# Performance work log

Measured on AMD Instinct MI355X. Metric: run time of the kernel, lower is better.

Reference implementation:

```python
import jax, jax.numpy as jnp
import numpy as np

N_HEAD, D_MODEL, D_K, D_V = 16, 1024, 64, 64
BIAS_WEIGHT = 1.0
NEG = -10000.0


def setup_inputs() -> dict:
    key = jax.random.key(0)
    ks = jax.random.split(key, 9)
    B, L = 2, 2048
    q = jax.random.normal(ks[0], (B, L, D_MODEL), dtype=jnp.float32)
    k = jax.random.normal(ks[1], (B, L, D_MODEL), dtype=jnp.float32)
    v = jax.random.normal(ks[2], (B, L, D_MODEL), dtype=jnp.float32)
    mask = jax.random.randint(ks[3], (B, L, L), 0, 2, dtype=jnp.int32)
    bias = jax.random.normal(ks[4], (B, L, L), dtype=jnp.float32)
    s = 1.0 / np.sqrt(D_MODEL)
    w_qs = jax.random.uniform(ks[5], (D_MODEL, N_HEAD * D_K), jnp.float32, -s, s)
    w_ks = jax.random.uniform(ks[6], (D_MODEL, N_HEAD * D_K), jnp.float32, -s, s)
    w_vs = jax.random.uniform(ks[7], (D_MODEL, N_HEAD * D_V), jnp.float32, -s, s)
    w_fc = jax.random.uniform(ks[8], (N_HEAD * D_V, D_MODEL), jnp.float32, -s, s)
    return {"q": q, "k": k, "v": v, "mask": mask, "bias": bias,
            "w_qs": w_qs, "w_ks": w_ks, "w_vs": w_vs, "w_fc": w_fc}


def reference(q, k, v, mask, bias, w_qs, w_ks, w_vs, w_fc):
    B, Lq, _ = q.shape
    # project and split heads: [B, H, L, d]
    qh = (q @ w_qs).reshape(B, Lq, N_HEAD, D_K).transpose(0, 2, 1, 3)
    kh = (k @ w_ks).reshape(B, k.shape[1], N_HEAD, D_K).transpose(0, 2, 1, 3)
    vh = (v @ w_vs).reshape(B, v.shape[1], N_HEAD, D_V).transpose(0, 2, 1, 3)
    temperature = D_K ** 0.5
    attn = jnp.einsum('bhqd,bhkd->bhqk', qh / temperature, kh)
    attn = attn + bias[:, None, :, :] * BIAS_WEIGHT
    attn = jnp.where(mask[:, None, :, :] == 0, NEG, attn)
    attn = jax.nn.softmax(attn, axis=-1)
    out = jnp.einsum('bhqk,bhkd->bhqd', attn, vh)
    out = out.transpose(0, 2, 1, 3).reshape(B, Lq, N_HEAD * D_V)
    return out @ w_fc
```

## Files before the change

kernel.cpp:

```cpp
#include <hip/hip_runtime.h>
#include <cstddef>

#define DEV static __device__ __forceinline__

typedef float f32x4 __attribute__((ext_vector_type(4)));
typedef __bf16 bf16x8 __attribute__((ext_vector_type(8)));
typedef __bf16 bf16x4v __attribute__((ext_vector_type(4)));
typedef unsigned short u16x8 __attribute__((ext_vector_type(8)));
typedef unsigned short u16x4 __attribute__((ext_vector_type(4)));
typedef unsigned u32x2 __attribute__((ext_vector_type(2)));
typedef unsigned u32x4 __attribute__((ext_vector_type(4)));
typedef _Float16 f16;
typedef _Float16 f16x4 __attribute__((ext_vector_type(4)));

constexpr int BB = 2, LL = 2048, DM = 1024, NH = 16, DK = 64;
constexpr float LOG2E = 1.44269504f;

DEV unsigned short f2bf(float f) {
  unsigned u = __builtin_bit_cast(unsigned, f);
  u += 0x7fffu + ((u >> 16) & 1u);
  return (unsigned short)(u >> 16);
}
DEV u16x4 cvt4(f32x4 v) {
  bf16x4v b = __builtin_convertvector(v, bf16x4v);
  return __builtin_bit_cast(u16x4, b);
}
DEV bf16x8 asbf(u16x8 v) { return __builtin_bit_cast(bf16x8, v); }
DEV f32x4 mfma16(u16x8 a, u16x8 b, f32x4 c) {
  return __builtin_amdgcn_mfma_f32_16x16x32_bf16(asbf(a), asbf(b), c, 0, 0, 0);
}
#if __has_builtin(__builtin_amdgcn_exp2f)
DEV float fexp2(float x) { return __builtin_amdgcn_exp2f(x); }
#else
DEV float fexp2(float x) { return exp2f(x); }
#endif
DEV void swap32(unsigned& a, unsigned& b) {
#if __has_builtin(__builtin_amdgcn_permlane32_swap)
  u32x2 r = __builtin_amdgcn_permlane32_swap(a, b, false, false);
  a = r[0]; b = r[1];
#else
  asm("v_permlane32_swap_b32 %0, %1" : "+v"(a), "+v"(b));
#endif
}
DEV void swap16(unsigned& a, unsigned& b) {
#if __has_builtin(__builtin_amdgcn_permlane16_swap)
  u32x2 r = __builtin_amdgcn_permlane16_swap(a, b, false, false);
  a = r[0]; b = r[1];
#else
  asm("v_permlane16_swap_b32 %0, %1" : "+v"(a), "+v"(b));
#endif
}
DEV void g2lds16(const void* g, void* l) {
  __builtin_amdgcn_global_load_lds(
      (const __attribute__((address_space(1))) unsigned int*)g,
      (__attribute__((address_space(3))) unsigned int*)l, 16, 0, 0);
}

__global__ __launch_bounds__(256) void prep_w(const float* __restrict__ w0,
                                              const float* __restrict__ w1,
                                              const float* __restrict__ w2,
                                              const float* __restrict__ w3,
                                              unsigned short* __restrict__ wT) {
  __shared__ float tile[32][33];
  int z = blockIdx.z;
  const float* W = (z == 0) ? w0 : (z == 1) ? w1 : (z == 2) ? w2 : w3;
  unsigned short* out = wT + (size_t)z * DM * DM;
  int k0 = blockIdx.y * 32, n0 = blockIdx.x * 32;
  int tx = threadIdx.x, ty = threadIdx.y;
#pragma unroll
  for (int p = 0; p < 4; p++)
    tile[ty + 8 * p][tx] = W[(size_t)(k0 + ty + 8 * p) * DM + n0 + tx];
  __syncthreads();
#pragma unroll
  for (int p = 0; p < 4; p++)
    out[(size_t)(n0 + ty + 8 * p) * DM + k0 + tx] = f2bf(tile[tx][ty + 8 * p]);
}

__global__ __launch_bounds__(256) void prep_bm(const int* __restrict__ mask,
                                               const float* __restrict__ bias,
                                               f16* __restrict__ bmf) {
  int t = threadIdx.x, w = t >> 6, lane = t & 63;
  int bq = blockIdx.y;
  int kt = blockIdx.x * 4 + w;
  int b = bq >> 7, qt = bq & 127;
  int q = qt * 16 + (lane & 15);
  int k = kt * 16 + (lane >> 4) * 4;
  size_t src = ((size_t)b * LL + q) * LL + k;
  int4 mk = *(const int4*)(mask + src);
  float4 bs = *(const float4*)(bias + src);
  f16x4 o;
  o[0] = (f16)((mk.x == 0 ? -10000.f : bs.x) * LOG2E);
  o[1] = (f16)((mk.y == 0 ? -10000.f : bs.y) * LOG2E);
  o[2] = (f16)((mk.z == 0 ? -10000.f : bs.z) * LOG2E);
  o[3] = (f16)((mk.w == 0 ? -10000.f : bs.w) * LOG2E);
  *(f16x4*)(bmf + ((size_t)bq * 128 + kt) * 256 + lane * 4) = o;
}

__global__ __launch_bounds__(256) void prep_cvt(const float* __restrict__ s0,
                                                const float* __restrict__ s1,
                                                const float* __restrict__ s2,
                                                unsigned short* __restrict__ dst) {
  int z = blockIdx.y;
  const float* src = (z == 0) ? s0 : (z == 1) ? s1 : s2;
  size_t i = ((size_t)blockIdx.x * 256 + threadIdx.x) * 8;
  float4 a = *(const float4*)(src + i);
  float4 b = *(const float4*)(src + i + 4);
  u16x8 o;
  o[0] = f2bf(a.x); o[1] = f2bf(a.y); o[2] = f2bf(a.z); o[3] = f2bf(a.w);
  o[4] = f2bf(b.x); o[5] = f2bf(b.y); o[6] = f2bf(b.z); o[7] = f2bf(b.w);
  *(u16x8*)(dst + (size_t)z * (size_t)(BB * LL) * DM + i) = o;
}

template <int KITERS>
DEV void gemm_core(const unsigned short* __restrict__ A,
                   const unsigned short* __restrict__ BT,
                   unsigned short (*Al)[128 * 64], unsigned short (*Bl)[128 * 64],
                   int m0, int n0, int k0beg, int t, f32x4 (&acc)[4][4]) {
  int lane = t & 63, c = lane & 15, qd = lane >> 4;
  int w = t >> 6, wm = w >> 1, wn = w & 1;
  int r0 = t >> 3;
  int gsw = (t & 7) ^ (r0 & 7);
  u16x8 ar[4], br[4];

  auto load_tile = [&](int k0) {
#pragma unroll
    for (int p = 0; p < 4; ++p) {
      ar[p] = *(const u16x8*)&A[(size_t)(m0 + 32 * p + r0) * DM + k0 + 8 * gsw];
      br[p] = *(const u16x8*)&BT[(size_t)(n0 + 32 * p + r0) * DM + k0 + 8 * gsw];
    }
  };
  auto store_tile = [&](int buf) {
#pragma unroll
    for (int p = 0; p < 4; ++p) {
      *(u16x8*)&Al[buf][p * 2048 + t * 8] = ar[p];
      *(u16x8*)&Bl[buf][p * 2048 + t * 8] = br[p];
    }
  };
  auto compute = [&](int buf) {
#pragma unroll
    for (int ks = 0; ks < 2; ++ks) {
      u16x8 af[4], bfr[4];
#pragma unroll
      for (int mt = 0; mt < 4; ++mt)
        af[mt] = *(const u16x8*)&Al[buf][(64 * wm + 16 * mt + c) * 64 +
                                         (((4 * ks + qd) ^ (c & 7)) << 3)];
#pragma unroll
      for (int nt = 0; nt < 4; ++nt)
        bfr[nt] = *(const u16x8*)&Bl[buf][(64 * wn + 16 * nt + c) * 64 +
                                          (((4 * ks + qd) ^ (c & 7)) << 3)];
#pragma unroll
      for (int mt = 0; mt < 4; ++mt)
#pragma unroll
        for (int nt = 0; nt < 4; ++nt)
          acc[mt][nt] = mfma16(af[mt], bfr[nt], acc[mt][nt]);
    }
  };

  load_tile(k0beg);
  store_tile(0);
  __syncthreads();
#pragma unroll 1
  for (int kk = 0; kk < KITERS; ++kk) {
    if (kk + 1 < KITERS) load_tile(k0beg + (kk + 1) * 64);
    compute(kk & 1);
    if (kk + 1 < KITERS) store_tile((kk + 1) & 1);
    __syncthreads();
  }
}

__global__ __launch_bounds__(256) void proj_gemm(const unsigned short* __restrict__ qkvb,
                                                 const unsigned short* __restrict__ wT,
                                                 unsigned short* __restrict__ qh,
                                                 unsigned short* __restrict__ kh,
                                                 unsigned short* __restrict__ vT) {
  __shared__ unsigned short Al[2][128 * 64];
  __shared__ unsigned short Bl[2][128 * 64];
  int z = blockIdx.z;
  const unsigned short* A = qkvb + (size_t)z * BB * LL * DM;
  const unsigned short* BT = wT + (size_t)z * DM * DM;
  int t = threadIdx.x, lane = t & 63, c = lane & 15, qd = lane >> 4;
  int w = t >> 6, wm = w >> 1, wn = w & 1;
  int m0 = blockIdx.y * 128, n0 = blockIdx.x * 128;
  f32x4 acc[4][4] = {};
  gemm_core<DM / 64>(A, BT, Al, Bl, m0, n0, 0, t, acc);

  if (z == 2) {
#pragma unroll
    for (int mt = 0; mt < 4; ++mt)
#pragma unroll
      for (int nt = 0; nt < 4; ++nt) {
        int n = n0 + 64 * wn + 16 * nt + c;
        int h = n >> 6, d = n & 63;
        int m = m0 + 64 * wm + 16 * mt + 4 * qd;
        int b = m >> 11, l = m & 2047;
        *(u16x4*)&vT[(((size_t)b * NH + h) * DK + d) * LL + l] = cvt4(acc[mt][nt]);
      }
  } else {
    unsigned short* Ch = z ? kh : qh;
    float scale = z ? 1.0f : 0.125f * LOG2E;
#pragma unroll
    for (int mt = 0; mt < 4; ++mt)
#pragma unroll
      for (int nt = 0; nt < 4; ++nt) {
        int n = n0 + 64 * wn + 16 * nt + c;
        int h = n >> 6, d = n & 63;
#pragma unroll
        for (int i = 0; i < 4; ++i) {
          int m = m0 + 64 * wm + 16 * mt + 4 * qd + i;
          int b = m >> 11, l = m & 2047;
          Ch[(((size_t)b * NH + h) * LL + l) * DK + d] = f2bf(acc[mt][nt][i] * scale);
        }
      }
  }
}

__global__ __launch_bounds__(256) void fc_gemm(const unsigned short* __restrict__ A,
                                               const unsigned short* __restrict__ BT,
                                               float* __restrict__ C) {
  __shared__ unsigned short Al[2][128 * 64];
  __shared__ unsigned short Bl[2][128 * 64];
  int t = threadIdx.x, lane = t & 63, c = lane & 15, qd = lane >> 4;
  int w = t >> 6, wm = w >> 1, wn = w & 1;
  int m0 = blockIdx.y * 128, n0 = blockIdx.x * 128;
  f32x4 acc[4][4] = {};
  gemm_core<8>(A, BT, Al, Bl, m0, n0, blockIdx.z * 512, t, acc);
#pragma unroll
  for (int mt = 0; mt < 4; ++mt)
#pragma unroll
    for (int nt = 0; nt < 4; ++nt) {
      int n = n0 + 64 * wn + 16 * nt + c;
#pragma unroll
      for (int i = 0; i < 4; ++i) {
        int m = m0 + 64 * wm + 16 * mt + 4 * qd + i;
        unsafeAtomicAdd(&C[(size_t)m * DM + n], acc[mt][nt][i]);
      }
    }
}

__global__ __launch_bounds__(256, 4) void attn_kern(
    const unsigned short* __restrict__ qh, const unsigned short* __restrict__ kh,
    const unsigned short* __restrict__ vT, const f16* __restrict__ bmf,
    unsigned short* __restrict__ O) {
  __shared__ unsigned short Kb[2][4096];
  __shared__ unsigned short Vb[2][4096];

  int t = threadIdx.x, w = t >> 6, lane = t & 63, c = lane & 15, qd = lane >> 4;
  int q0 = blockIdx.x * 64, h = blockIdx.y, b = blockIdx.z;
  const unsigned short* Q = qh + (((size_t)b * NH + h) * LL + q0) * DK;
  const unsigned short* K = kh + ((size_t)b * NH + h) * LL * DK;
  const unsigned short* V = vT + ((size_t)b * NH + h) * DK * LL;
  const f16* BMF = bmf + (((size_t)b * 128 + blockIdx.x * 4 + w) * 128) * 256 +
                   lane * 4;
  int rt = t >> 3, gg = t & 7;

#pragma unroll
  for (int r = 0; r < 2; ++r) {
    int row = r * 32 + rt;
    int sc = ((gg ^ (row & 7)) << 3);
    g2lds16(&Q[(size_t)row * DK + sc], &Kb[1][r * 2048 + w * 512]);
    g2lds16(&K[(size_t)row * DK + sc], &Kb[0][r * 2048 + w * 512]);
    g2lds16(&V[(size_t)row * LL + sc], &Vb[0][r * 2048 + w * 512]);
  }
  f16x4 bA[4], bB[4];
#pragma unroll
  for (int mt = 0; mt < 4; ++mt) bA[mt] = *(const f16x4*)&BMF[(size_t)mt * 256];
  __syncthreads();

  u16x8 qf[2];
#pragma unroll
  for (int ks = 0; ks < 2; ++ks)
    qf[ks] = *(const u16x8*)&Kb[1][(16 * w + c) * 64 +
                                   (((4 * ks + qd) ^ (c & 7)) << 3)];
  __syncthreads();

  float li = 0.f;
  f32x4 oacc[4] = {};

  auto body = [&](int it, f16x4 (&bc)[4], f16x4 (&bn)[4]) {
    int cur = it & 1;
    const unsigned short* Kl = Kb[cur];
    const unsigned short* Vt = Vb[cur];
    if (it + 1 < 32) {
      int nb = cur ^ 1, kt1 = (it + 1) * 64;
#pragma unroll
      for (int r = 0; r < 2; ++r) {
        int row = r * 32 + rt;
        int sc = ((gg ^ (row & 7)) << 3);
        g2lds16(&K[(size_t)(kt1 + row) * DK + sc], &Kb[nb][r * 2048 + w * 512]);
        g2lds16(&V[(size_t)row * LL + kt1 + sc], &Vb[nb][r * 2048 + w * 512]);
      }
#pragma unroll
      for (int mt = 0; mt < 4; ++mt)
        bn[mt] = *(const f16x4*)&BMF[(size_t)((it + 1) * 4 + mt) * 256];
    }

    f32x4 s[4];
#pragma unroll
    for (int mt = 0; mt < 4; ++mt) {
      int row = 16 * mt + c;
      u16x8 k0f = *(const u16x8*)&Kl[row * 64 + ((qd ^ (c & 7)) << 3)];
      u16x8 k1f = *(const u16x8*)&Kl[row * 64 + (((4 + qd) ^ (c & 7)) << 3)];
      f32x4 z = {0.f, 0.f, 0.f, 0.f};
      z = mfma16(k0f, qf[0], z);
      s[mt] = mfma16(k1f, qf[1], z);
    }
    u16x8 pf[2];
    {
      unsigned L[4], H[4];
#pragma unroll
      for (int mt = 0; mt < 4; ++mt) {
        f16x4 b4 = bc[mt];
        f32x4 p;
#pragma unroll
        for (int i = 0; i < 4; ++i) {
          p[i] = fexp2(s[mt][i] + (float)b4[i]);
          li += p[i];
        }
        u32x2 lw = __builtin_bit_cast(u32x2, cvt4(p));
        L[mt] = lw[0];
        H[mt] = lw[1];
      }
#pragma unroll
      for (int ks = 0; ks < 2; ++ks) {
        unsigned l0 = L[2 * ks], l1 = L[2 * ks + 1];
        unsigned h0 = H[2 * ks], h1 = H[2 * ks + 1];
        swap32(l0, l1); swap16(l0, l1);
        swap32(h0, h1); swap16(h0, h1);
        u32x4 pw = {l0, h0, l1, h1};
        pf[ks] = __builtin_bit_cast(u16x8, pw);
      }
    }
#pragma unroll
    for (int dt = 0; dt < 4; ++dt) {
      int row = 16 * dt + c;
      u16x8 v0f = *(const u16x8*)&Vt[row * 64 + ((qd ^ (c & 7)) << 3)];
      u16x8 v1f = *(const u16x8*)&Vt[row * 64 + (((4 + qd) ^ (c & 7)) << 3)];
      oacc[dt] = mfma16(v0f, pf[0], oacc[dt]);
      oacc[dt] = mfma16(v1f, pf[1], oacc[dt]);
    }
    __syncthreads();
  };

#pragma unroll 1
  for (int it = 0; it < 32; it += 2) {
    body(it, bA, bB);
    body(it + 1, bB, bA);
  }

  {
    float l = li;
    l += __shfl_xor(l, 16);
    l += __shfl_xor(l, 32);
    float rl = 1.f / l;
    size_t orow = ((size_t)b * LL + q0 + 16 * w + c) * DM + h * DK;
#pragma unroll
    for (int dt = 0; dt < 4; ++dt)
      *(u16x4*)&O[orow + 16 * dt + 4 * qd] = cvt4(oacc[dt] * rl);
  }
}

extern "C" void kernel_launch(void* const* d_in, const int* in_sizes, int n_in,
                              void* d_out, int out_size, void* d_ws, size_t ws_size,
                              hipStream_t stream) {
  (void)in_sizes; (void)n_in; (void)ws_size;
  const float* q = (const float*)d_in[0];
  const float* k = (const float*)d_in[1];
  const float* v = (const float*)d_in[2];
  const int* mask = (const int*)d_in[3];
  const float* bias = (const float*)d_in[4];
  const float* w_qs = (const float*)d_in[5];
  const float* w_ks = (const float*)d_in[6];
  const float* w_vs = (const float*)d_in[7];
  const float* w_fc = (const float*)d_in[8];

  char* ws = (char*)d_ws;
  const size_t MB = 1024 * 1024;
  unsigned short* wT = (unsigned short*)(ws);
  f16* bmf = (f16*)(ws + 8 * MB);
  unsigned short* qkvb = (unsigned short*)(ws + 24 * MB);
  unsigned short* qh = (unsigned short*)(ws + 48 * MB);
  unsigned short* kh = (unsigned short*)(ws + 56 * MB);
  unsigned short* vhT = (unsigned short*)(ws + 64 * MB);
  unsigned short* Obuf = (unsigned short*)(ws + 72 * MB);

  prep_w<<<dim3(32, 32, 4), dim3(32, 8, 1), 0, stream>>>(w_qs, w_ks, w_vs, w_fc, wT);
  prep_bm<<<dim3(32, 256), dim3(256), 0, stream>>>(mask, bias, bmf);
  prep_cvt<<<dim3(2048, 3), dim3(256), 0, stream>>>(q, k, v, qkvb);
  proj_gemm<<<dim3(8, 32, 3), 256, 0, stream>>>(qkvb, wT, qh, kh, vhT);
  attn_kern<<<dim3(32, 16, 2), 256, 0, stream>>>(qh, kh, vhT, bmf, Obuf);
  hipMemsetAsync(d_out, 0, (size_t)out_size * sizeof(float), stream);
  fc_gemm<<<dim3(8, 32, 2), 256, 0, stream>>>(Obuf, wT + (size_t)3 * DM * DM,
                                              (float*)d_out);
}
```

Baseline: 308.8 us.

## Fuse prep kernels and memset, use direct-to-LDS GEMM loads, MFMA rowsum

Merges the three preprocessing kernels and the output memset into one launch, which removes launch gaps. The GEMM core switches from register-staged double buffering to single-buffered global_load_lds with halved LDS and a 3-block occupancy hint, so there is less register traffic but also less load/compute overlap. The attention kernel computes the softmax denominator with an MFMA against a ones vector instead of scalar adds and shuffles, and raises wave priority around the MFMA sections.

```diff
diff --git a/kernel.cpp b/kernel.cpp
--- a/kernel.cpp
+++ b/kernel.cpp
@@ -56,125 +56,112 @@
       (__attribute__((address_space(3))) unsigned int*)l, 16, 0, 0);
 }
 
-__global__ __launch_bounds__(256) void prep_w(const float* __restrict__ w0,
-                                              const float* __restrict__ w1,
-                                              const float* __restrict__ w2,
-                                              const float* __restrict__ w3,
-                                              unsigned short* __restrict__ wT) {
-  __shared__ float tile[32][33];
-  int z = blockIdx.z;
-  const float* W = (z == 0) ? w0 : (z == 1) ? w1 : (z == 2) ? w2 : w3;
-  unsigned short* out = wT + (size_t)z * DM * DM;
-  int k0 = blockIdx.y * 32, n0 = blockIdx.x * 32;
-  int tx = threadIdx.x, ty = threadIdx.y;
-#pragma unroll
-  for (int p = 0; p < 4; p++)
-    tile[ty + 8 * p][tx] = W[(size_t)(k0 + ty + 8 * p) * DM + n0 + tx];
-  __syncthreads();
-#pragma unroll
-  for (int p = 0; p < 4; p++)
-    out[(size_t)(n0 + ty + 8 * p) * DM + k0 + tx] = f2bf(tile[tx][ty + 8 * p]);
-}
-
-__global__ __launch_bounds__(256) void prep_bm(const int* __restrict__ mask,
-                                               const float* __restrict__ bias,
-                                               f16* __restrict__ bmf) {
-  int t = threadIdx.x, w = t >> 6, lane = t & 63;
-  int bq = blockIdx.y;
-  int kt = blockIdx.x * 4 + w;
-  int b = bq >> 7, qt = bq & 127;
-  int q = qt * 16 + (lane & 15);
-  int k = kt * 16 + (lane >> 4) * 4;
-  size_t src = ((size_t)b * LL + q) * LL + k;
-  int4 mk = *(const int4*)(mask + src);
-  float4 bs = *(const float4*)(bias + src);
-  f16x4 o;
-  o[0] = (f16)((mk.x == 0 ? -10000.f : bs.x) * LOG2E);
-  o[1] = (f16)((mk.y == 0 ? -10000.f : bs.y) * LOG2E);
-  o[2] = (f16)((mk.z == 0 ? -10000.f : bs.z) * LOG2E);
-  o[3] = (f16)((mk.w == 0 ? -10000.f : bs.w) * LOG2E);
-  *(f16x4*)(bmf + ((size_t)bq * 128 + kt) * 256 + lane * 4) = o;
-}
-
-__global__ __launch_bounds__(256) void prep_cvt(const float* __restrict__ s0,
-                                                const float* __restrict__ s1,
-                                                const float* __restrict__ s2,
-                                                unsigned short* __restrict__ dst) {
-  int z = blockIdx.y;
-  const float* src = (z == 0) ? s0 : (z == 1) ? s1 : s2;
-  size_t i = ((size_t)blockIdx.x * 256 + threadIdx.x) * 8;
-  float4 a = *(const float4*)(src + i);
-  float4 b = *(const float4*)(src + i + 4);
-  u16x8 o;
-  o[0] = f2bf(a.x); o[1] = f2bf(a.y); o[2] = f2bf(a.z); o[3] = f2bf(a.w);
-  o[4] = f2bf(b.x); o[5] = f2bf(b.y); o[6] = f2bf(b.z); o[7] = f2bf(b.w);
-  *(u16x8*)(dst + (size_t)z * (size_t)(BB * LL) * DM + i) = o;
+__global__ __launch_bounds__(256) void prep_all(
+    const float* __restrict__ w0, const float* __restrict__ w1,
+    const float* __restrict__ w2, const float* __restrict__ w3,
+    unsigned short* __restrict__ wT, const int* __restrict__ mask,
+    const float* __restrict__ bias, f16* __restrict__ bmf,
+    const float* __restrict__ s0, const float* __restrict__ s1,
+    const float* __restrict__ s2, unsigned short* __restrict__ qkvb,
+    float* __restrict__ dout) {
+  int f = blockIdx.x, t = threadIdx.x;
+  if (f < 4096) {
+    __shared__ float tile[32][33];
+    int z = f >> 10, rem = f & 1023;
+    int k0 = (rem >> 5) * 32, n0 = (rem & 31) * 32;
+    const float* W = (z == 0) ? w0 : (z == 1) ? w1 : (z == 2) ? w2 : w3;
+    unsigned short* out = wT + (size_t)z * DM * DM;
+    int tx = t & 31, ty = t >> 5;
+#pragma unroll
+    for (int p = 0; p < 4; p++)
+      tile[ty + 8 * p][tx] = W[(size_t)(k0 + ty + 8 * p) * DM + n0 + tx];
+    __syncthreads();
+#pragma unroll
+    for (int p = 0; p < 4; p++)
+      out[(size_t)(n0 + ty + 8 * p) * DM + k0 + tx] = f2bf(tile[tx][ty + 8 * p]);
+  } else if (f < 12288) {
+    int f2 = f - 4096;
+    int w = t >> 6, lane = t & 63;
+    int bq = f2 >> 5;
+    int kt = (f2 & 31) * 4 + w;
+    int b = bq >> 7, qt = bq & 127;
+    int q = qt * 16 + (lane & 15);
+    int k = kt * 16 + (lane >> 4) * 4;
+    size_t src = ((size_t)b * LL + q) * LL + k;
+    int4 mk = *(const int4*)(mask + src);
+    float4 bs = *(const float4*)(bias + src);
+    f16x4 o;
+    o[0] = (f16)((mk.x == 0 ? -10000.f : bs.x) * LOG2E);
+    o[1] = (f16)((mk.y == 0 ? -10000.f : bs.y) * LOG2E);
+    o[2] = (f16)((mk.z == 0 ? -10000.f : bs.z) * LOG2E);
+    o[3] = (f16)((mk.w == 0 ? -10000.f : bs.w) * LOG2E);
+    *(f16x4*)(bmf + ((size_t)bq * 128 + kt) * 256 + lane * 4) = o;
+  } else if (f < 18432) {
+    int f3 = f - 12288;
+    int z = f3 >> 11;
+    const float* src = (z == 0) ? s0 : (z == 1) ? s1 : s2;
+    size_t i = ((size_t)(f3 & 2047) * 256 + t) * 8;
+    float4 a = *(const float4*)(src + i);
+    float4 b = *(const float4*)(src + i + 4);
+    u16x8 o;
+    o[0] = f2bf(a.x); o[1] = f2bf(a.y); o[2] = f2bf(a.z); o[3] = f2bf(a.w);
+    o[4] = f2bf(b.x); o[5] = f2bf(b.y); o[6] = f2bf(b.z); o[7] = f2bf(b.w);
+    *(u16x8*)(qkvb + (size_t)z * (size_t)(BB * LL) * DM + i) = o;
+  } else {
+    size_t i = ((size_t)(f - 18432) * 256 + t) * 4;
+    float4 zz = {0.f, 0.f, 0.f, 0.f};
+    *(float4*)(dout + i) = zz;
+  }
 }
 
 template <int KITERS>
 DEV void gemm_core(const unsigned short* __restrict__ A,
                    const unsigned short* __restrict__ BT,
-                   unsigned short (*Al)[128 * 64], unsigned short (*Bl)[128 * 64],
+                   unsigned short* Al, unsigned short* Bl,
                    int m0, int n0, int k0beg, int t, f32x4 (&acc)[4][4]) {
   int lane = t & 63, c = lane & 15, qd = lane >> 4;
   int w = t >> 6, wm = w >> 1, wn = w & 1;
   int r0 = t >> 3;
   int gsw = (t & 7) ^ (r0 & 7);
-  u16x8 ar[4], br[4];
-
-  auto load_tile = [&](int k0) {
+
+#pragma unroll 1
+  for (int kk = 0; kk < KITERS; ++kk) {
+    int k0 = k0beg + kk * 64;
 #pragma unroll
     for (int p = 0; p < 4; ++p) {
-      ar[p] = *(const u16x8*)&A[(size_t)(m0 + 32 * p + r0) * DM + k0 + 8 * gsw];
-      br[p] = *(const u16x8*)&BT[(size_t)(n0 + 32 * p + r0) * DM + k0 + 8 * gsw];
-    }
-  };
-  auto store_tile = [&](int buf) {
-#pragma unroll
-    for (int p = 0; p < 4; ++p) {
-      *(u16x8*)&Al[buf][p * 2048 + t * 8] = ar[p];
-      *(u16x8*)&Bl[buf][p * 2048 + t * 8] = br[p];
-    }
-  };
-  auto compute = [&](int buf) {
+      g2lds16(&A[(size_t)(m0 + 32 * p + r0) * DM + k0 + 8 * gsw],
+              &Al[p * 2048 + w * 512]);
+      g2lds16(&BT[(size_t)(n0 + 32 * p + r0) * DM + k0 + 8 * gsw],
+              &Bl[p * 2048 + w * 512]);
+    }
+    __syncthreads();
 #pragma unroll
     for (int ks = 0; ks < 2; ++ks) {
       u16x8 af[4], bfr[4];
 #pragma unroll
       for (int mt = 0; mt < 4; ++mt)
-        af[mt] = *(const u16x8*)&Al[buf][(64 * wm + 16 * mt + c) * 64 +
-                                         (((4 * ks + qd) ^ (c & 7)) << 3)];
+        af[mt] = *(const u16x8*)&Al[(64 * wm + 16 * mt + c) * 64 +
+                                    (((4 * ks + qd) ^ (c & 7)) << 3)];
 #pragma unroll
       for (int nt = 0; nt < 4; ++nt)
-        bfr[nt] = *(const u16x8*)&Bl[buf][(64 * wn + 16 * nt + c) * 64 +
-                                          (((4 * ks + qd) ^ (c & 7)) << 3)];
+        bfr[nt] = *(const u16x8*)&Bl[(64 * wn + 16 * nt + c) * 64 +
+                                     (((4 * ks + qd) ^ (c & 7)) << 3)];
 #pragma unroll
       for (int mt = 0; mt < 4; ++mt)
 #pragma unroll
         for (int nt = 0; nt < 4; ++nt)
           acc[mt][nt] = mfma16(af[mt], bfr[nt], acc[mt][nt]);
     }
-  };
-
-  load_tile(k0beg);
-  store_tile(0);
-  __syncthreads();
-#pragma unroll 1
-  for (int kk = 0; kk < KITERS; ++kk) {
-    if (kk + 1 < KITERS) load_tile(k0beg + (kk + 1) * 64);
-    compute(kk & 1);
-    if (kk + 1 < KITERS) store_tile((kk + 1) & 1);
     __syncthreads();
   }
 }
 
-__global__ __launch_bounds__(256) void proj_gemm(const unsigned short* __restrict__ qkvb,
-                                                 const unsigned short* __restrict__ wT,
-                                                 unsigned short* __restrict__ qh,
-                                                 unsigned short* __restrict__ kh,
-                                                 unsigned short* __restrict__ vT) {
-  __shared__ unsigned short Al[2][128 * 64];
-  __shared__ unsigned short Bl[2][128 * 64];
+__global__ __launch_bounds__(256, 3) void proj_gemm(
+    const unsigned short* __restrict__ qkvb, const unsigned short* __restrict__ wT,
+    unsigned short* __restrict__ qh, unsigned short* __restrict__ kh,
+    unsigned short* __restrict__ vT) {
+  __shared__ unsigned short Al[128 * 64];
+  __shared__ unsigned short Bl[128 * 64];
   int z = blockIdx.z;
   const unsigned short* A = qkvb + (size_t)z * BB * LL * DM;
   const unsigned short* BT = wT + (size_t)z * DM * DM;
@@ -214,11 +201,11 @@
   }
 }
 
-__global__ __launch_bounds__(256) void fc_gemm(const unsigned short* __restrict__ A,
-                                               const unsigned short* __restrict__ BT,
-                                               float* __restrict__ C) {
-  __shared__ unsigned short Al[2][128 * 64];
-  __shared__ unsigned short Bl[2][128 * 64];
+__global__ __launch_bounds__(256, 3) void fc_gemm(const unsigned short* __restrict__ A,
+                                                  const unsigned short* __restrict__ BT,
+                                                  float* __restrict__ C) {
+  __shared__ unsigned short Al[128 * 64];
+  __shared__ unsigned short Bl[128 * 64];
   int t = threadIdx.x, lane = t & 63, c = lane & 15, qd = lane >> 4;
   int w = t >> 6, wm = w >> 1, wn = w & 1;
   int m0 = blockIdx.y * 128, n0 = blockIdx.x * 128;
@@ -273,7 +260,9 @@
                                    (((4 * ks + qd) ^ (c & 7)) << 3)];
   __syncthreads();
 
-  float li = 0.f;
+  const u16x8 ones = {0x3F80, 0x3F80, 0x3F80, 0x3F80,
+                      0x3F80, 0x3F80, 0x3F80, 0x3F80};
+  f32x4 lacc = {};
   f32x4 oacc[4] = {};
 
   auto body = [&](int it, f16x4 (&bc)[4], f16x4 (&bn)[4]) {
@@ -295,6 +284,7 @@
     }
 
     f32x4 s[4];
+    __builtin_amdgcn_s_setprio(1);
 #pragma unroll
     for (int mt = 0; mt < 4; ++mt) {
       int row = 16 * mt + c;
@@ -304,6 +294,7 @@
       z = mfma16(k0f, qf[0], z);
       s[mt] = mfma16(k1f, qf[1], z);
     }
+    __builtin_amdgcn_s_setprio(0);
     u16x8 pf[2];
     {
       unsigned L[4], H[4];
@@ -312,10 +303,7 @@
         f16x4 b4 = bc[mt];
         f32x4 p;
 #pragma unroll
-        for (int i = 0; i < 4; ++i) {
-          p[i] = fexp2(s[mt][i] + (float)b4[i]);
-          li += p[i];
-        }
+        for (int i = 0; i < 4; ++i) p[i] = fexp2(s[mt][i] + (float)b4[i]);
         u32x2 lw = __builtin_bit_cast(u32x2, cvt4(p));
         L[mt] = lw[0];
         H[mt] = lw[1];
@@ -330,6 +318,9 @@
         pf[ks] = __builtin_bit_cast(u16x8, pw);
       }
     }
+    __builtin_amdgcn_s_setprio(1);
+    lacc = mfma16(ones, pf[0], lacc);
+    lacc = mfma16(ones, pf[1], lacc);
 #pragma unroll
     for (int dt = 0; dt < 4; ++dt) {
       int row = 16 * dt + c;
@@ -338,6 +329,7 @@
       oacc[dt] = mfma16(v0f, pf[0], oacc[dt]);
       oacc[dt] = mfma16(v1f, pf[1], oacc[dt]);
     }
+    __builtin_amdgcn_s_setprio(0);
     __syncthreads();
   };
 
@@ -348,10 +340,7 @@
   }
 
   {
-    float l = li;
-    l += __shfl_xor(l, 16);
-    l += __shfl_xor(l, 32);
-    float rl = 1.f / l;
+    float rl = 1.f / lacc[0];
     size_t orow = ((size_t)b * LL + q0 + 16 * w + c) * DM + h * DK;
 #pragma unroll
     for (int dt = 0; dt < 4; ++dt)
@@ -362,7 +351,7 @@
 extern "C" void kernel_launch(void* const* d_in, const int* in_sizes, int n_in,
                               void* d_out, int out_size, void* d_ws, size_t ws_size,
                               hipStream_t stream) {
-  (void)in_sizes; (void)n_in; (void)ws_size;
+  (void)in_sizes; (void)n_in; (void)ws_size; (void)out_size;
   const float* q = (const float*)d_in[0];
   const float* k = (const float*)d_in[1];
   const float* v = (const float*)d_in[2];
@@ -383,12 +372,11 @@
   unsigned short* vhT = (unsigned short*)(ws + 64 * MB);
   unsigned short* Obuf = (unsigned short*)(ws + 72 * MB);
 
-  prep_w<<<dim3(32, 32, 4), dim3(32, 8, 1), 0, stream>>>(w_qs, w_ks, w_vs, w_fc, wT);
-  prep_bm<<<dim3(32, 256), dim3(256), 0, stream>>>(mask, bias, bmf);
-  prep_cvt<<<dim3(2048, 3), dim3(256), 0, stream>>>(q, k, v, qkvb);
+  prep_all<<<dim3(22528), dim3(256), 0, stream>>>(w_qs, w_ks, w_vs, w_fc, wT,
+                                                  mask, bias, bmf, q, k, v, qkvb,
+                                                  (float*)d_out);
   proj_gemm<<<dim3(8, 32, 3), 256, 0, stream>>>(qkvb, wT, qh, kh, vhT);
   attn_kern<<<dim3(32, 16, 2), 256, 0, stream>>>(qh, kh, vhT, bmf, Obuf);
-  hipMemsetAsync(d_out, 0, (size_t)out_size * sizeof(float), stream);
   fc_gemm<<<dim3(8, 32, 2), 256, 0, stream>>>(Obuf, wT + (size_t)3 * DM * DM,
                                               (float*)d_out);
 }
```

After: 294.4 us. 4.7% less time.
